# Optimization experiments

Measured on AMD Instinct MI355X. Metric: run time of the kernel, lower is better.

## Reference

```python
import jax, jax.numpy as jnp
import numpy as np

L = 8192   # sequence length
B = 4      # batch
D = 512    # embed_dim
NDIM = 16  # EMA state dim
Z = 128    # shared q/k dim
W = 128    # attention window
MP = 256   # max relative positions
NEG = -50000.0  # TOKEN_SELF_ATTN_VALUE-style mask fill


def setup_inputs() -> dict:
    key = jax.random.key(0)
    ks = jax.random.split(key, 16)
    def tn(k, shp, std):  # truncated-normal-ish init (clipped normal)
        return jnp.clip(jax.random.normal(k, shp) * std, -2 * std, 2 * std)
    val = jnp.ones((NDIM, 1)).at[1::2].set(-1.0)  # MultiHeadEMA beta init pattern
    return {
        "x": jax.random.normal(ks[0], (L, B, D), dtype=jnp.float32),
        "delta": tn(ks[1], (D, NDIM, 1), 0.2),
        "alpha": tn(ks[2], (D, NDIM, 1), 0.2),
        "beta": tn(ks[3], (D, NDIM, 1), 0.02) + val,
        "gamma": jax.random.normal(ks[4], (D, NDIM)),
        "omega": jax.random.normal(ks[5], (D,)),
        "Wp": tn(ks[6], (D, 1), 0.02),      # LatentConfigurator weight_proj
        "bp": jnp.zeros((1,)),
        "temp": jnp.array([0.5 * np.log(D)], dtype=jnp.float32),  # log(sqrt(D))
        "Wz": tn(ks[7], (D, Z), 0.02),
        "qg": jax.random.normal(ks[8], (Z,)) * 0.02 + 1.0,
        "qb": jnp.zeros((Z,)),
        "kg": jax.random.normal(ks[9], (Z,)) * 0.02 + 1.0,
        "kb": jnp.zeros((Z,)),
        "Wv": tn(ks[10], (D, D), 0.02),
        "relb": tn(ks[11], (2 * MP - 1,), 0.02),  # FastRelativePositionalBias table
    }


def _rotary(t, cos, sin):
    # t: (B, L, Z); cos/sin: (L, Z//2). Complex rotation on interleaved pairs.
    t1, t2 = t[..., 0::2], t[..., 1::2]
    return jnp.stack([t1 * cos - t2 * sin, t1 * sin + t2 * cos], axis=-1).reshape(t.shape)


def _forward(x, delta, alpha, beta, gamma, omega, Wp, bp, temp, Wz, qg, qb, kg, kb, Wv, relb):
    scale = 1.0 / np.sqrt(NDIM)
    # ---- MultiHeadEMA: damped EMA as long convolution via FFT ----
    p = jax.nn.sigmoid(delta)                      # (D,N,1)
    a = jax.nn.sigmoid(alpha)
    logq = jnp.log1p(-(p * a))                     # log(1 - p*alpha)
    t = jnp.arange(L, dtype=jnp.float32)
    kern = (p * beta) * jnp.exp(logq * t)          # (D,N,L) Vandermonde kernel
    k1d = jnp.einsum('dnl,dn->dl', kern, gamma * scale)  # (D,L)
    xb = x.transpose(1, 2, 0)                      # (B,D,L)
    conv = jnp.fft.irfft(jnp.fft.rfft(xb, n=2 * L) * jnp.fft.rfft(k1d, n=2 * L), n=2 * L)[..., :L]
    mx = jax.nn.silu(conv.transpose(2, 0, 1) + x * omega)  # (L,B,D)
    # ---- LatentConfigurator: sigmoid token routing (proj_dim==1) ----
    pi = jax.nn.sigmoid((mx @ Wp + bp) / jnp.exp(temp))[..., 0].T  # (B,L)
    mxb = mx.transpose(1, 0, 2)                    # (B,L,D)
    sel = pi > 0.5
    idx = jnp.cumsum(sel.astype(jnp.int32), axis=1) * sel  # (B,L); 0 -> dropped slot
    counts = sel.sum(axis=1)                       # (B,)
    bi = jnp.arange(B)[:, None]
    # compress_seq: scatter selected tokens to compact prefix (slot 0 dropped)
    c = jnp.zeros((B, L + 1, D), mx.dtype).at[bi, idx].add(mxb * sel[..., None])[:, 1:]
    # ---- windowed attention over compressed tokens ----
    z = jax.nn.silu(c @ Wz)                        # (B,L,Z)
    freqs = 1.0 / (10000.0 ** (jnp.arange(0, Z, 2, dtype=jnp.float32) / Z))
    ang = jnp.arange(L, dtype=jnp.float32)[:, None] * freqs
    cos, sin = jnp.cos(ang), jnp.sin(ang)
    q = _rotary(z * qg + qb, cos, sin)
    kk = _rotary(z * kg + kb, cos, sin)
    v = jax.nn.silu(c @ Wv)                        # (B,L,D)
    n = L // W
    qw = q.reshape(B, n, W, Z)
    def look_around(tw):  # prepend previous window: (B,n,W,f) -> (B,n,2W,f)
        prev = jnp.pad(tw, ((0, 0), (1, 0), (0, 0), (0, 0)))[:, :-1]
        return jnp.concatenate([prev, tw], axis=2)
    kw = look_around(kk.reshape(B, n, W, Z))
    vw = look_around(v.reshape(B, n, W, D))
    base = (jnp.arange(n) * W)[:, None, None]
    qabs = base + jnp.arange(W)[None, :, None]         # (n,W,1)
    kabs = base + jnp.arange(-W, W)[None, None, :]     # (n,1,2W)
    mask = (kabs <= qabs) & (kabs >= 0) & (kabs[None] < counts[:, None, None, None])  # (B,n,W,2W)
    rel = jnp.arange(-W, W)[None, :] - jnp.arange(W)[:, None]   # (W,2W)
    bias = relb[jnp.clip(rel + MP - 1, 0, 2 * MP - 2)]          # (W,2W)
    scores = jnp.einsum('bnwz,bnkz->bnwk', qw, kw) / np.sqrt(Z) + bias
    attn = jax.nn.softmax(jnp.where(mask, scores, NEG), axis=-1)
    h = jnp.einsum('bnwk,bnkd->bnwd', attn, vw).reshape(B, L, D)
    # ---- extract: gather back to original positions, gate by pi ----
    hpad = jnp.concatenate([jnp.zeros((B, 1, D), h.dtype), h], axis=1)
    hsel = jnp.take_along_axis(hpad, idx[..., None], axis=1)    # (B,L,D)
    return x + (hsel * pi[..., None]).transpose(1, 0, 2)        # (L,B,D)


def reference(x, delta, alpha, beta, gamma, omega, Wp, bp, temp, Wz, qg, qb, kg, kb, Wv, relb):
    return _forward(x, delta, alpha, beta, gamma, omega, Wp, bp, temp, Wz, qg, qb, kg, kb, Wv, relb)
```

## Files before the change

### kernel.cpp

```cpp
#include <hip/hip_runtime.h>
#include <math.h>

constexpr int L = 8192;
constexpr int B = 4;
constexpr int D = 512;
constexpr int NDIM = 16;
constexpr int Z = 128;
constexpr float NEGF = -50000.0f;
constexpr int CCL = 64;
constexpr int NCH = L / CCL;
constexpr int FMAX = 64;

typedef short s16x8 __attribute__((ext_vector_type(8)));
typedef float f32x4 __attribute__((ext_vector_type(4)));

typedef __attribute__((address_space(1))) const void* as1cv;
typedef __attribute__((address_space(3))) void* as3v;

__device__ __forceinline__ void gld16(const void* g, void* l) {
  __builtin_amdgcn_global_load_lds((as1cv)g, (as3v)l, 16, 0, 0);
}

__device__ __forceinline__ unsigned short f2bf(float f) {
  unsigned u = __builtin_bit_cast(unsigned, f);
  u += 0x7fffu + ((u >> 16) & 1u);
  return (unsigned short)(u >> 16);
}

__global__ __launch_bounds__(256) void k_prep(const float* __restrict__ delta,
                                              const float* __restrict__ alpha,
                                              const float* __restrict__ beta,
                                              const float* __restrict__ gamma,
                                              double* __restrict__ qdn,
                                              double* __restrict__ cdn,
                                              double* __restrict__ rp1,
                                              double* __restrict__ rp2,
                                              float* __restrict__ qf,
                                              float* __restrict__ cf,
                                              float* __restrict__ r1f,
                                              float* __restrict__ r2f,
                                              int* __restrict__ fcnt) {
  int i = blockIdx.x * 256 + threadIdx.x;
  if (i == 0) *fcnt = 0;
  if (i >= D * NDIM) return;
  double p = 1.0 / (1.0 + exp(-(double)delta[i]));
  double a = 1.0 / (1.0 + exp(-(double)alpha[i]));
  double q = 1.0 - p * a;
  double c = p * (double)beta[i] * (double)gamma[i] * 0.25;
  qdn[i] = q; cdn[i] = c;
  double q2 = q * q, q4 = q2 * q2, q8 = q4 * q4;
  double q16 = q8 * q8, q32 = q16 * q16, q64 = q32 * q32;
  rp1[i] = q64;
  rp2[i] = q64 * q64;
  qf[i] = (float)q; cf[i] = (float)c;
  r1f[i] = (float)q64; r2f[i] = (float)(q64 * q64);
}

__global__ __launch_bounds__(256) void k_convA(const float* __restrict__ x,
                                               const float* __restrict__ qf,
                                               float* __restrict__ E) {
  int bx = blockIdx.x;
  int tile = bx & 31, dg = (bx >> 5) & 7, b = bx >> 8;
  int dl = threadIdx.x & 63, cl = threadIdx.x >> 6;
  int dgl = dg * 64 + dl;
  int t = tile * 4 + cl;
  float q[NDIM], s[NDIM];
#pragma unroll
  for (int n = 0; n < NDIM; ++n) { q[n] = qf[dgl * NDIM + n]; s[n] = 0.f; }
  const float* xp = x + ((size_t)(t * CCL) * B + b) * D + dgl;
#pragma unroll 4
  for (int i = 0; i < CCL; ++i) {
    float xv = xp[i * (B * D)];
#pragma unroll
    for (int n = 0; n < NDIM; ++n) s[n] = fmaf(q[n], s[n], xv);
  }
  float* eb = E + ((size_t)(b * NCH + t) * NDIM) * 512 + dgl;
#pragma unroll
  for (int n = 0; n < NDIM; ++n) eb[(size_t)n * 512] = s[n];
}

__global__ __launch_bounds__(256) void k_convC(const float* __restrict__ x,
                                               const float* __restrict__ omega,
                                               const float* __restrict__ qf,
                                               const float* __restrict__ cf,
                                               const float* __restrict__ r1f,
                                               const float* __restrict__ r2f,
                                               const float* __restrict__ E,
                                               const float* __restrict__ Wp,
                                               unsigned short* __restrict__ mxb,
                                               float* __restrict__ pdot) {
  int bx = blockIdx.x;
  int tile = bx & 31, dg = (bx >> 5) & 7, b = bx >> 8;
  int dl = threadIdx.x & 63, cl = threadIdx.x >> 6;
  int dgl = dg * 64 + dl;
  int t = tile * 4 + cl;
  float q[NDIM], c[NDIM], s[NDIM];
#pragma unroll
  for (int n = 0; n < NDIM; ++n) {
    q[n] = qf[dgl * NDIM + n];
    c[n] = cf[dgl * NDIM + n];
    s[n] = 0.f;
  }
  if (t >= 1) {
    const float* e1 = E + ((size_t)(b * NCH + t - 1) * NDIM) * 512 + dgl;
#pragma unroll
    for (int n = 0; n < NDIM; ++n) s[n] = e1[(size_t)n * 512];
  }
  if (t >= 2) {
    const float* e2 = E + ((size_t)(b * NCH + t - 2) * NDIM) * 512 + dgl;
#pragma unroll
    for (int n = 0; n < NDIM; ++n) s[n] = fmaf(r1f[dgl * NDIM + n], e2[(size_t)n * 512], s[n]);
  }
  if (t >= 3) {
    const float* e3 = E + ((size_t)(b * NCH + t - 3) * NDIM) * 512 + dgl;
#pragma unroll
    for (int n = 0; n < NDIM; ++n) s[n] = fmaf(r2f[dgl * NDIM + n], e3[(size_t)n * 512], s[n]);
  }
  float om = omega[dgl];
  float wp = Wp[dgl];
  const float* xp = x + ((size_t)(t * CCL) * B + b) * D + dgl;
  unsigned short* mp = mxb + ((size_t)b * L + t * CCL) * 512 + dgl;
  float* pp = pdot + ((size_t)(b * L + t * CCL)) * 8 + dg;
  for (int i = 0; i < CCL; ++i) {
    float xv = xp[i * (B * D)];
#pragma unroll
    for (int n = 0; n < NDIM; ++n) s[n] = fmaf(q[n], s[n], xv);
    float p0 = c[0] * s[0], p1 = c[1] * s[1], p2 = c[2] * s[2], p3 = c[3] * s[3];
    p0 = fmaf(c[4], s[4], p0);  p1 = fmaf(c[5], s[5], p1);
    p2 = fmaf(c[6], s[6], p2);  p3 = fmaf(c[7], s[7], p3);
    p0 = fmaf(c[8], s[8], p0);  p1 = fmaf(c[9], s[9], p1);
    p2 = fmaf(c[10], s[10], p2); p3 = fmaf(c[11], s[11], p3);
    p0 = fmaf(c[12], s[12], p0); p1 = fmaf(c[13], s[13], p1);
    p2 = fmaf(c[14], s[14], p2); p3 = fmaf(c[15], s[15], p3);
    float conv = (p0 + p1) + (p2 + p3);
    float m = fmaf(xv, om, conv);
    float v = m / (1.0f + __expf(-m));
    mp[(size_t)i * 512] = f2bf(v);
    float pd = v * wp;
#pragma unroll
    for (int off = 32; off; off >>= 1) pd += __shfl_down(pd, off, 64);
    if (dl == 0) pp[(size_t)i * 8] = pd;
  }
}

__global__ __launch_bounds__(256) void k_logitc(const float* __restrict__ pdot,
                                                const float* __restrict__ bp,
                                                const float* __restrict__ temp,
                                                float* __restrict__ pi,
                                                int* __restrict__ selb,
                                                int* __restrict__ fcnt,
                                                int* __restrict__ flags) {
  int rid = blockIdx.x * 256 + threadIdx.x;
  const float* pr = pdot + (size_t)rid * 8;
  double acc = 0.0;
#pragma unroll
  for (int j = 0; j < 8; ++j) acc += (double)pr[j];
  double logit = acc + (double)bp[0];
  pi[rid] = (float)(1.0 / (1.0 + exp(-logit / exp((double)temp[0]))));
  selb[rid] = (logit > 0.0) ? 1 : 0;
  if (fabs(logit) < 1e-4) {
    int slot = atomicAdd(fcnt, 1);
    if (slot < FMAX) flags[slot] = rid;
  }
}

__global__ __launch_bounds__(256) void k_fix(const int* __restrict__ fcnt,
                                             const int* __restrict__ flags,
                                             const float* __restrict__ x,
                                             const double* __restrict__ qdn,
                                             const double* __restrict__ cdn,
                                             const double* __restrict__ rp1,
                                             const double* __restrict__ rp2,
                                             const float* __restrict__ omega,
                                             const float* __restrict__ Wp,
                                             double* __restrict__ pfix) {
  int nb = blockIdx.x;
  int fi = nb >> 3, dblk = nb & 7;
  int count = *fcnt; if (count > FMAX) count = FMAX;
  if (fi >= count) return;
  int rid = flags[fi];
  int b = rid >> 13, l = rid & (L - 1);
  int t = l >> 6, io = l & 63;
  int sub = threadIdx.x >> 6, dl = threadIdx.x & 63;
  int d = dblk * 64 + dl;
  double q[NDIM], s[NDIM];
#pragma unroll
  for (int n = 0; n < NDIM; ++n) { q[n] = qdn[d * NDIM + n]; s[n] = 0.0; }
  int c0 = (sub < 3) ? (t - 3 + sub) : t;
  int steps = (sub < 3) ? 64 : (io + 1);
  if (c0 >= 0) {
    const float* xp = x + ((size_t)(c0 * CCL) * B + b) * D + d;
    for (int i = 0; i < steps; ++i) {
      double xv = (double)xp[(size_t)i * (B * D)];
#pragma unroll
      for (int n = 0; n < NDIM; ++n) s[n] = fma(q[n], s[n], xv);
    }
  }
  __shared__ double Esm[4][64][NDIM];
#pragma unroll
  for (int n = 0; n < NDIM; ++n) Esm[sub][dl][n] = s[n];
  __syncthreads();
  if (sub == 3) {
    double sfin[NDIM];
#pragma unroll
    for (int n = 0; n < NDIM; ++n) {
      double base = q[n], r = 1.0;
      int e = io + 1;
      while (e) { if (e & 1) r *= base; base *= base; e >>= 1; }
      double S = Esm[2][dl][n] + rp1[d * NDIM + n] * Esm[1][dl][n] + rp2[d * NDIM + n] * Esm[0][dl][n];
      sfin[n] = Esm[3][dl][n] + r * S;
    }
    double conv = 0.0;
#pragma unroll
    for (int n = 0; n < NDIM; ++n) conv = fma(cdn[d * NDIM + n], sfin[n], conv);
    double xv = (double)x[((size_t)l * B + b) * D + d];
    double m = conv + xv * (double)omega[d];
    double mxd = m / (1.0 + exp(-m));
    double v = mxd * (double)Wp[d];
#pragma unroll
    for (int off = 32; off; off >>= 1) v += __shfl_down(v, off, 64);
    if (dl == 0) pfix[fi * 8 + dblk] = v;
  }
}

__global__ __launch_bounds__(64) void k_fix2(const int* __restrict__ fcnt,
                                             const int* __restrict__ flags,
                                             const double* __restrict__ pfix,
                                             const float* __restrict__ bp,
                                             const float* __restrict__ temp,
                                             float* __restrict__ pi,
                                             int* __restrict__ selb) {
  int fi = threadIdx.x;
  int count = *fcnt; if (count > FMAX) count = FMAX;
  if (fi >= count) return;
  double s = 0.0;
#pragma unroll
  for (int j = 0; j < 8; ++j) s += pfix[fi * 8 + j];
  double logit = s + (double)bp[0];
  int rid = flags[fi];
  selb[rid] = (logit > 0.0) ? 1 : 0;
  pi[rid] = (float)(1.0 / (1.0 + exp(-logit / exp((double)temp[0]))));
}

__global__ __launch_bounds__(256) void k_scan(const int* __restrict__ selb,
                                              int* __restrict__ idx,
                                              int* __restrict__ src,
                                              int* __restrict__ counts) {
  int b = blockIdx.x;
  int t = threadIdx.x;
  __shared__ int part[256];
  const int PER = L / 256;
  int base = b * L + t * PER;
  int loc[PER];
  int cnt = 0;
#pragma unroll
  for (int i = 0; i < PER; ++i) { loc[i] = selb[base + i]; cnt += loc[i]; }
  part[t] = cnt;
  __syncthreads();
  for (int off = 1; off < 256; off <<= 1) {
    int v = (t >= off) ? part[t - off] : 0;
    __syncthreads();
    part[t] += v;
    __syncthreads();
  }
  int run = (t == 0) ? 0 : part[t - 1];
#pragma unroll
  for (int i = 0; i < PER; ++i) {
    int sflag = loc[i];
    run += sflag;
    idx[base + i] = sflag ? run : 0;
    if (sflag) src[b * L + run - 1] = t * PER + i;
  }
  if (t == 255) counts[b] = part[255];
}

__global__ __launch_bounds__(256) void k_buildc(const unsigned short* __restrict__ mxb,
                                                const int* __restrict__ src,
                                                const int* __restrict__ counts,
                                                unsigned short* __restrict__ c) {
  int row = blockIdx.x * 4 + (threadIdx.x >> 6);
  int lane = threadIdx.x & 63;
  int b = row >> 13;
  int j = row & (L - 1);
  s16x8 o = {0, 0, 0, 0, 0, 0, 0, 0};
  if (j < counts[b])
    o = *(const s16x8*)(mxb + ((size_t)b * L + src[row]) * 512 + lane * 8);
  *(s16x8*)(c + (size_t)row * D + lane * 8) = o;
}

__global__ __launch_bounds__(256) void k_wt(const float* __restrict__ Wm,
                                            unsigned short* __restrict__ Wt, int N) {
  int idx = blockIdx.x * 256 + threadIdx.x;
  int n = idx >> 9, kk = idx & 511;
  Wt[idx] = f2bf(Wm[(size_t)kk * N + n]);
}

__global__ __launch_bounds__(256) void k_gemm_mfma(const unsigned short* __restrict__ A,
                                                   const unsigned short* __restrict__ Bt,
                                                   float* __restrict__ outF,
                                                   unsigned short* __restrict__ outT,
                                                   int N, int mode) {
  __shared__ char As[16384];
  __shared__ char Bs[16384];
  int tid = threadIdx.x;
  int w = tid >> 6, l = tid & 63;
  int m0 = blockIdx.x * 128, n0 = blockIdx.y * 128;
  int wr = w >> 1, wc = w & 1;
  f32x4 acc[4][4];
  f32x4 zz = {0.f, 0.f, 0.f, 0.f};
#pragma unroll
  for (int mi = 0; mi < 4; ++mi)
#pragma unroll
    for (int ni = 0; ni < 4; ++ni) acc[mi][ni] = zz;

  for (int k0 = 0; k0 < 512; k0 += 64) {
#pragma unroll
    for (int ld = 0; ld < 4; ++ld) {
      int li = w * 4 + ld;
      int row = li * 8 + (l >> 3);
      int col = (((l & 7) ^ (row & 7)) << 3);
      gld16(A + (size_t)(m0 + row) * 512 + k0 + col, As + li * 1024);
      gld16(Bt + (size_t)(n0 + row) * 512 + k0 + col, Bs + li * 1024);
    }
    __syncthreads();
    s16x8 af[4][2], bfr[4][2];
#pragma unroll
    for (int kh = 0; kh < 2; ++kh) {
#pragma unroll
      for (int mi = 0; mi < 4; ++mi) {
        int row = wr * 64 + mi * 16 + (l & 15);
        int byte = row * 128 + ((kh * 64 + ((l >> 4) * 16)) ^ ((row & 7) << 4));
        af[mi][kh] = *(const s16x8*)(As + byte);
      }
#pragma unroll
      for (int ni = 0; ni < 4; ++ni) {
        int row = wc * 64 + ni * 16 + (l & 15);
        int byte = row * 128 + ((kh * 64 + ((l >> 4) * 16)) ^ ((row & 7) << 4));
        bfr[ni][kh] = *(const s16x8*)(Bs + byte);
      }
    }
#pragma unroll
    for (int kh = 0; kh < 2; ++kh)
#pragma unroll
      for (int mi = 0; mi < 4; ++mi)
#pragma unroll
        for (int ni = 0; ni < 4; ++ni)
          acc[mi][ni] = __builtin_amdgcn_mfma_f32_16x16x32_bf16(af[mi][kh], bfr[ni][kh], acc[mi][ni], 0, 0, 0);
    __syncthreads();
  }
#pragma unroll
  for (int mi = 0; mi < 4; ++mi)
#pragma unroll
    for (int ni = 0; ni < 4; ++ni)
#pragma unroll
      for (int r = 0; r < 4; ++r) {
        float vv = acc[mi][ni][r];
        vv = vv / (1.0f + __expf(-vv));
        int mrow = m0 + wr * 64 + mi * 16 + (l >> 4) * 4 + r;
        int ncol = n0 + wc * 64 + ni * 16 + (l & 15);
        if (mode == 0) {
          outF[(size_t)mrow * N + ncol] = vv;
        } else {
          int b = mrow >> 13, j = mrow & 8191;
          outT[((size_t)(b * 512 + ncol)) * 8192 + j] = f2bf(vv);
        }
      }
}

__global__ __launch_bounds__(256) void k_rot(const float* __restrict__ z,
                                             const float* __restrict__ qg,
                                             const float* __restrict__ qb,
                                             const float* __restrict__ kg,
                                             const float* __restrict__ kb,
                                             unsigned short* __restrict__ qo,
                                             unsigned short* __restrict__ ko) {
  int tid = blockIdx.x * 256 + threadIdx.x;
  int i = tid & 63;
  int row = tid >> 6;
  int j = row & (L - 1);
  double freq = exp(((double)(-2 * i) / 128.0) * log(10000.0));
  float angf = (float)j * (float)freq;
  double sa, ca;
  sincos((double)angf, &sa, &ca);
  float cc = (float)ca, ss = (float)sa;
  size_t base = (size_t)row * Z + 2 * i;
  float z1 = z[base], z2 = z[base + 1];
  float q1 = z1 * qg[2 * i] + qb[2 * i], q2 = z2 * qg[2 * i + 1] + qb[2 * i + 1];
  float k1 = z1 * kg[2 * i] + kb[2 * i], k2 = z2 * kg[2 * i + 1] + kb[2 * i + 1];
  qo[base]     = f2bf(q1 * cc - q2 * ss);
  qo[base + 1] = f2bf(q1 * ss + q2 * cc);
  ko[base]     = f2bf(k1 * cc - k2 * ss);
  ko[base + 1] = f2bf(k1 * ss + k2 * cc);
}

__global__ __launch_bounds__(512) void k_attn_mfma(const unsigned short* __restrict__ q,
                                                   const unsigned short* __restrict__ k,
                                                   const unsigned short* __restrict__ vT,
                                                   const float* __restrict__ relb,
                                                   const int* __restrict__ counts,
                                                   float* __restrict__ h) {
  __shared__ char smem[131072];
  char* Qs = smem;
  char* Ks = smem + 32768;
  char* Ps = smem;
  char* Vs = smem + 65536;
  int tid = threadIdx.x, w = tid >> 6, l = tid & 63;
  int n = blockIdx.x & 63, b = blockIdx.x >> 6;
  int cnt = counts[b];
  int q0 = n * 128, kbase = q0 - 128;
  const size_t rowb = (size_t)b * L;

#pragma unroll
  for (int ld = 0; ld < 4; ++ld) {
    int li = w * 4 + ld;
    int row = li * 4 + (l >> 4);
    int colb = ((l & 15) * 16) ^ ((row & 7) << 4);
    gld16((const char*)(q + (rowb + q0 + row) * Z) + colb, Qs + li * 1024);
  }
#pragma unroll
  for (int ld = 0; ld < 8; ++ld) {
    int li = w * 8 + ld;
    int row = li * 4 + (l >> 4);
    int jk = kbase + row; if (jk < 0) jk = 0;
    int colb = ((l & 15) * 16) ^ ((row & 7) << 4);
    gld16((const char*)(k + (rowb + jk) * Z) + colb, Ks + li * 1024);
  }
  __syncthreads();

  int m0 = w * 16;
  f32x4 s[16];
  f32x4 zz = {0.f, 0.f, 0.f, 0.f};
#pragma unroll
  for (int ni = 0; ni < 16; ++ni) s[ni] = zz;
  s16x8 aq[4];
#pragma unroll
  for (int ks = 0; ks < 4; ++ks) {
    int row = m0 + (l & 15);
    int byte = row * 256 + ((ks * 64 + ((l >> 4) * 16)) ^ ((row & 7) << 4));
    aq[ks] = *(const s16x8*)(Qs + byte);
  }
#pragma unroll
  for (int ni = 0; ni < 16; ++ni) {
    int row = ni * 16 + (l & 15);
    int rb = row * 256, sw = (row & 7) << 4;
#pragma unroll
    for (int ks = 0; ks < 4; ++ks) {
      s16x8 bk = *(const s16x8*)(Ks + rb + ((ks * 64 + ((l >> 4) * 16)) ^ sw));
      s[ni] = __builtin_amdgcn_mfma_f32_16x16x32_bf16(aq[ks], bk, s[ni], 0, 0, 0);
    }
  }
  __syncthreads();

  auto stageV = [&](int nc) {
#pragma unroll
    for (int ld = 0; ld < 8; ++ld) {
      int li = w * 8 + ld;
      int row = li * 2 + (l >> 5);
      int colb = ((l & 31) * 16) ^ ((row & 7) << 4);
      int j = kbase + (colb >> 1);
      if (j < 0) j = 0;
      gld16((const char*)(vT + ((size_t)(b * 512 + nc * 128 + row)) * L + j), Vs + li * 1024);
    }
  };
  stageV(0);

  int rgrp = (l >> 4) * 4;
  float mxr[4] = {-3e38f, -3e38f, -3e38f, -3e38f};
#pragma unroll
  for (int ni = 0; ni < 16; ++ni) {
    int col = ni * 16 + (l & 15);
    int kabs = kbase + col;
#pragma unroll
    for (int r = 0; r < 4; ++r) {
      int ww = m0 + rgrp + r;
      bool valid = (kabs >= 0) && (kabs <= q0 + ww) && (kabs < cnt);
      float vv = valid ? (s[ni][r] * 0.08838834764831845f + relb[col + 127 - ww]) : NEGF;
      s[ni][r] = vv;
      mxr[r] = fmaxf(mxr[r], vv);
    }
  }
#pragma unroll
  for (int r = 0; r < 4; ++r)
    for (int off = 1; off < 16; off <<= 1)
      mxr[r] = fmaxf(mxr[r], __shfl_xor(mxr[r], off, 64));
  float smr[4] = {0.f, 0.f, 0.f, 0.f};
#pragma unroll
  for (int ni = 0; ni < 16; ++ni)
#pragma unroll
    for (int r = 0; r < 4; ++r) {
      float p = __expf(s[ni][r] - mxr[r]);
      s[ni][r] = p;
      smr[r] += p;
    }
#pragma unroll
  for (int r = 0; r < 4; ++r) {
    for (int off = 1; off < 16; off <<= 1) smr[r] += __shfl_xor(smr[r], off, 64);
    smr[r] = 1.0f / smr[r];
  }
#pragma unroll
  for (int ni = 0; ni < 16; ++ni) {
    int colb2 = (ni * 16 + (l & 15)) * 2;
#pragma unroll
    for (int r = 0; r < 4; ++r) {
      int row = m0 + rgrp + r;
      *(unsigned short*)(Ps + row * 512 + (colb2 ^ ((row & 7) << 4))) = f2bf(s[ni][r] * smr[r]);
    }
  }
  __syncthreads();

  for (int nc = 0; nc < 4; ++nc) {
    if (nc) {
      __syncthreads();
      stageV(nc);
      __syncthreads();
    }
    f32x4 o[8];
#pragma unroll
    for (int ni = 0; ni < 8; ++ni) o[ni] = zz;
    int prow = m0 + (l & 15);
    int psw = (prow & 7) << 4;
#pragma unroll
    for (int kt = 0; kt < 4; ++kt) {
      s16x8 pa0 = *(const s16x8*)(Ps + prow * 512 + ((kt * 128 + ((l >> 4) * 16)) ^ psw));
      s16x8 pa1 = *(const s16x8*)(Ps + prow * 512 + ((kt * 128 + 64 + ((l >> 4) * 16)) ^ psw));
#pragma unroll
      for (int ni = 0; ni < 8; ++ni) {
        int vrow = ni * 16 + (l & 15);
        int vsw = (vrow & 7) << 4;
        s16x8 vb0 = *(const s16x8*)(Vs + vrow * 512 + ((kt * 128 + ((l >> 4) * 16)) ^ vsw));
        s16x8 vb1 = *(const s16x8*)(Vs + vrow * 512 + ((kt * 128 + 64 + ((l >> 4) * 16)) ^ vsw));
        o[ni] = __builtin_amdgcn_mfma_f32_16x16x32_bf16(pa0, vb0, o[ni], 0, 0, 0);
        o[ni] = __builtin_amdgcn_mfma_f32_16x16x32_bf16(pa1, vb1, o[ni], 0, 0, 0);
      }
    }
#pragma unroll
    for (int ni = 0; ni < 8; ++ni)
#pragma unroll
      for (int r = 0; r < 4; ++r)
        h[(rowb + q0 + m0 + rgrp + r) * 512 + nc * 128 + ni * 16 + (l & 15)] = o[ni][r];
  }
}

__global__ __launch_bounds__(256) void k_final(const float* __restrict__ x,
                                               const float* __restrict__ h,
                                               const float* __restrict__ pi,
                                               const int* __restrict__ idx,
                                               float* __restrict__ out) {
  int e4 = blockIdx.x * 256 + threadIdx.x;
  int dq = e4 & 127;
  int rem = e4 >> 7;
  int b = rem & 3;
  int l = rem >> 2;
  float4 xv = ((const float4*)x)[e4];
  int ix = idx[(b << 13) + l];
  if (ix > 0) {
    float pv = pi[(b << 13) + l];
    float4 hv = ((const float4*)(h + ((size_t)(b << 13) + ix - 1) * 512))[dq];
    xv.x += hv.x * pv; xv.y += hv.y * pv;
    xv.z += hv.z * pv; xv.w += hv.w * pv;
  }
  ((float4*)out)[e4] = xv;
}

extern "C" void kernel_launch(void* const* d_in, const int* in_sizes, int n_in,
                              void* d_out, int out_size, void* d_ws, size_t ws_size,
                              hipStream_t stream) {
  const float* x     = (const float*)d_in[0];
  const float* delta = (const float*)d_in[1];
  const float* alpha = (const float*)d_in[2];
  const float* beta  = (const float*)d_in[3];
  const float* gamma = (const float*)d_in[4];
  const float* omega = (const float*)d_in[5];
  const float* Wp    = (const float*)d_in[6];
  const float* bp    = (const float*)d_in[7];
  const float* temp  = (const float*)d_in[8];
  const float* Wz    = (const float*)d_in[9];
  const float* qg    = (const float*)d_in[10];
  const float* qb    = (const float*)d_in[11];
  const float* kg    = (const float*)d_in[12];
  const float* kb    = (const float*)d_in[13];
  const float* Wv    = (const float*)d_in[14];
  const float* relb  = (const float*)d_in[15];
  (void)in_sizes; (void)n_in; (void)out_size; (void)ws_size;

  char* wsb = (char*)d_ws;
  size_t o = 0;
  auto alloc = [&](size_t bytes) {
    char* p = wsb + o;
    o += (bytes + 255) & ~(size_t)255;
    return p;
  };
  float* hbuf          = (float*)alloc((size_t)B * L * D * 4);
  unsigned short* mxb  = (unsigned short*)hbuf;
  char*  eAndCb        = alloc((size_t)B * L * D * 2);
  float* Ebuf          = (float*)eAndCb;
  unsigned short* cb   = (unsigned short*)eAndCb;
  float* zb            = (float*)alloc((size_t)B * L * Z * 4);
  unsigned short* qb2  = (unsigned short*)alloc((size_t)B * L * Z * 2);
  unsigned short* kb2  = (unsigned short*)alloc((size_t)B * L * Z * 2);
  unsigned short* vTb  = (unsigned short*)alloc((size_t)B * D * L * 2);
  unsigned short* wzt  = (unsigned short*)alloc((size_t)Z * 512 * 2);
  unsigned short* wvt  = (unsigned short*)alloc((size_t)D * 512 * 2);
  float* pdot = (float*)alloc((size_t)B * L * 8 * 4);
  float* pib  = (float*)alloc((size_t)B * L * 4);
  int* selb   = (int*)alloc((size_t)B * L * 4);
  int* idx    = (int*)alloc((size_t)B * L * 4);
  int* src    = (int*)alloc((size_t)B * L * 4);
  int* cnt    = (int*)alloc(256);
  double* qdn = (double*)alloc((size_t)D * NDIM * 8);
  double* cdn = (double*)alloc((size_t)D * NDIM * 8);
  double* rp1 = (double*)alloc((size_t)D * NDIM * 8);
  double* rp2 = (double*)alloc((size_t)D * NDIM * 8);
  float* qf   = (float*)alloc((size_t)D * NDIM * 4);
  float* cf   = (float*)alloc((size_t)D * NDIM * 4);
  float* r1f  = (float*)alloc((size_t)D * NDIM * 4);
  float* r2f  = (float*)alloc((size_t)D * NDIM * 4);
  int* fcnt   = (int*)alloc(256);
  int* flags  = (int*)alloc(FMAX * 4);
  double* pfix = (double*)alloc((size_t)FMAX * 8 * 8);

  k_prep<<<(D * NDIM + 255) / 256, 256, 0, stream>>>(delta, alpha, beta, gamma,
                                                     qdn, cdn, rp1, rp2, qf, cf, r1f, r2f, fcnt);
  k_convA<<<B * 8 * 32, 256, 0, stream>>>(x, qf, Ebuf);
  k_convC<<<B * 8 * 32, 256, 0, stream>>>(x, omega, qf, cf, r1f, r2f, Ebuf, Wp, mxb, pdot);
  k_logitc<<<B * L / 256, 256, 0, stream>>>(pdot, bp, temp, pib, selb, fcnt, flags);
  k_fix<<<FMAX * 8, 256, 0, stream>>>(fcnt, flags, x, qdn, cdn, rp1, rp2, omega, Wp, pfix);
  k_fix2<<<1, 64, 0, stream>>>(fcnt, flags, pfix, bp, temp, pib, selb);
  k_scan<<<B, 256, 0, stream>>>(selb, idx, src, cnt);
  k_buildc<<<B * L / 4, 256, 0, stream>>>(mxb, src, cnt, cb);
  k_wt<<<Z * 512 / 256, 256, 0, stream>>>(Wz, wzt, Z);
  k_wt<<<D * 512 / 256, 256, 0, stream>>>(Wv, wvt, D);
  k_gemm_mfma<<<dim3(256, 1), 256, 0, stream>>>(cb, wzt, zb, vTb, Z, 0);
  k_gemm_mfma<<<dim3(256, 4), 256, 0, stream>>>(cb, wvt, zb, vTb, D, 1);
  k_rot<<<B * L * (Z / 2) / 256, 256, 0, stream>>>(zb, qg, qb, kg, kb, qb2, kb2);
  k_attn_mfma<<<B * 64, 512, 0, stream>>>(qb2, kb2, vTb, relb, cnt, hbuf);
  k_final<<<(int)((size_t)L * B * D / 4 / 256), 256, 0, stream>>>(x, hbuf, pib, idx, (float*)d_out);
}
```

Before: 272.2 us.

## Fuse gather into GEMM, tabulate rotary, DPP reduction, LDS-transposed stores

Removes the k_buildc gather kernel and its intermediate buffer. The GEMM now loads A rows directly from mxb through the src index, and k_scan zero-fills the unused src entries. The transposed bf16 V output is staged through swizzled LDS so global writes are 16-byte coalesced. Rotary cos/sin are computed once per position in a small table kernel instead of a double-precision sincos per batch element. The per-step 64-lane shuffle reduction in convC becomes a DPP reduction, with an unroll added. Padded rows now compute on real row-0 data instead of zeros, which is safe only if those rows stay masked downstream.

Result: faster. 230.2 us (-15.4%).

```diff
diff --git a/kernel.cpp b/kernel.cpp
--- a/kernel.cpp
+++ b/kernel.cpp
@@ -26,6 +26,13 @@
   u += 0x7fffu + ((u >> 16) & 1u);
   return (unsigned short)(u >> 16);
 }
+
+#define DPPADD(acc, ctrl, rmask)                                                   \
+  {                                                                                \
+    int _mv = __builtin_amdgcn_update_dpp(0, __builtin_bit_cast(int, acc),         \
+                                          ctrl, rmask, 0xf, false);                \
+    acc += __builtin_bit_cast(float, _mv);                                         \
+  }
 
 __global__ __launch_bounds__(256) void k_prep(const float* __restrict__ delta,
                                               const float* __restrict__ alpha,
@@ -56,6 +63,17 @@
   r1f[i] = (float)q64; r2f[i] = (float)(q64 * q64);
 }
 
+__global__ __launch_bounds__(256) void k_tab(float2* __restrict__ tab) {
+  int tid = blockIdx.x * 256 + threadIdx.x;
+  int i = tid & 63, j = tid >> 6;
+  double freq = exp(((double)(-2 * i) / 128.0) * log(10000.0));
+  float angf = (float)j * (float)freq;
+  double sa, ca;
+  sincos((double)angf, &sa, &ca);
+  float2 r; r.x = (float)ca; r.y = (float)sa;
+  tab[tid] = r;
+}
+
 __global__ __launch_bounds__(256) void k_convA(const float* __restrict__ x,
                                                const float* __restrict__ qf,
                                                float* __restrict__ E) {
@@ -121,6 +139,7 @@
   const float* xp = x + ((size_t)(t * CCL) * B + b) * D + dgl;
   unsigned short* mp = mxb + ((size_t)b * L + t * CCL) * 512 + dgl;
   float* pp = pdot + ((size_t)(b * L + t * CCL)) * 8 + dg;
+#pragma unroll 4
   for (int i = 0; i < CCL; ++i) {
     float xv = xp[i * (B * D)];
 #pragma unroll
@@ -137,9 +156,13 @@
     float v = m / (1.0f + __expf(-m));
     mp[(size_t)i * 512] = f2bf(v);
     float pd = v * wp;
-#pragma unroll
-    for (int off = 32; off; off >>= 1) pd += __shfl_down(pd, off, 64);
-    if (dl == 0) pp[(size_t)i * 8] = pd;
+    DPPADD(pd, 0x111, 0xf);
+    DPPADD(pd, 0x112, 0xf);
+    DPPADD(pd, 0x114, 0xf);
+    DPPADD(pd, 0x118, 0xf);
+    DPPADD(pd, 0x142, 0xa);
+    DPPADD(pd, 0x143, 0x8);
+    if (dl == 63) pp[(size_t)i * 8] = pd;
   }
 }
 
@@ -272,20 +295,9 @@
     if (sflag) src[b * L + run - 1] = t * PER + i;
   }
   if (t == 255) counts[b] = part[255];
-}
-
-__global__ __launch_bounds__(256) void k_buildc(const unsigned short* __restrict__ mxb,
-                                                const int* __restrict__ src,
-                                                const int* __restrict__ counts,
-                                                unsigned short* __restrict__ c) {
-  int row = blockIdx.x * 4 + (threadIdx.x >> 6);
-  int lane = threadIdx.x & 63;
-  int b = row >> 13;
-  int j = row & (L - 1);
-  s16x8 o = {0, 0, 0, 0, 0, 0, 0, 0};
-  if (j < counts[b])
-    o = *(const s16x8*)(mxb + ((size_t)b * L + src[row]) * 512 + lane * 8);
-  *(s16x8*)(c + (size_t)row * D + lane * 8) = o;
+  __syncthreads();
+  int total = part[255];
+  for (int i2 = total + t; i2 < L; i2 += 256) src[b * L + i2] = 0;
 }
 
 __global__ __launch_bounds__(256) void k_wt(const float* __restrict__ Wm,
@@ -295,17 +307,31 @@
   Wt[idx] = f2bf(Wm[(size_t)kk * N + n]);
 }
 
-__global__ __launch_bounds__(256) void k_gemm_mfma(const unsigned short* __restrict__ A,
+__global__ __launch_bounds__(256) void k_gemm_mfma(const unsigned short* __restrict__ mxb,
+                                                   const int* __restrict__ src,
                                                    const unsigned short* __restrict__ Bt,
                                                    float* __restrict__ outF,
                                                    unsigned short* __restrict__ outT,
                                                    int N, int mode) {
-  __shared__ char As[16384];
-  __shared__ char Bs[16384];
+  __shared__ char smem[32768];
+  char* As = smem;
+  char* Bs = smem + 16384;
   int tid = threadIdx.x;
   int w = tid >> 6, l = tid & 63;
   int m0 = blockIdx.x * 128, n0 = blockIdx.y * 128;
+  int gb = m0 >> 13, j0 = m0 & 8191;
   int wr = w >> 1, wc = w & 1;
+  const unsigned short* arow[4];
+  const unsigned short* brow[4];
+#pragma unroll
+  for (int ld = 0; ld < 4; ++ld) {
+    int li = w * 4 + ld;
+    int row = li * 8 + (l >> 3);
+    int col = ((l & 7) ^ (row & 7)) << 3;
+    int srow = src[gb * 8192 + j0 + row];
+    arow[ld] = mxb + ((size_t)gb * 8192 + srow) * 512 + col;
+    brow[ld] = Bt + (size_t)(n0 + row) * 512 + col;
+  }
   f32x4 acc[4][4];
   f32x4 zz = {0.f, 0.f, 0.f, 0.f};
 #pragma unroll
@@ -317,10 +343,8 @@
 #pragma unroll
     for (int ld = 0; ld < 4; ++ld) {
       int li = w * 4 + ld;
-      int row = li * 8 + (l >> 3);
-      int col = (((l & 7) ^ (row & 7)) << 3);
-      gld16(A + (size_t)(m0 + row) * 512 + k0 + col, As + li * 1024);
-      gld16(Bt + (size_t)(n0 + row) * 512 + k0 + col, Bs + li * 1024);
+      gld16(arow[ld] + k0, As + li * 1024);
+      gld16(brow[ld] + k0, Bs + li * 1024);
     }
     __syncthreads();
     s16x8 af[4][2], bfr[4][2];
@@ -348,26 +372,49 @@
           acc[mi][ni] = __builtin_amdgcn_mfma_f32_16x16x32_bf16(af[mi][kh], bfr[ni][kh], acc[mi][ni], 0, 0, 0);
     __syncthreads();
   }
-#pragma unroll
-  for (int mi = 0; mi < 4; ++mi)
-#pragma unroll
-    for (int ni = 0; ni < 4; ++ni)
-#pragma unroll
-      for (int r = 0; r < 4; ++r) {
-        float vv = acc[mi][ni][r];
-        vv = vv / (1.0f + __expf(-vv));
-        int mrow = m0 + wr * 64 + mi * 16 + (l >> 4) * 4 + r;
-        int ncol = n0 + wc * 64 + ni * 16 + (l & 15);
-        if (mode == 0) {
+  if (mode == 0) {
+#pragma unroll
+    for (int mi = 0; mi < 4; ++mi)
+#pragma unroll
+      for (int ni = 0; ni < 4; ++ni)
+#pragma unroll
+        for (int r = 0; r < 4; ++r) {
+          float vv = acc[mi][ni][r];
+          vv = vv / (1.0f + __expf(-vv));
+          int mrow = m0 + wr * 64 + mi * 16 + (l >> 4) * 4 + r;
+          int ncol = n0 + wc * 64 + ni * 16 + (l & 15);
           outF[(size_t)mrow * N + ncol] = vv;
-        } else {
-          int b = mrow >> 13, j = mrow & 8191;
-          outT[((size_t)(b * 512 + ncol)) * 8192 + j] = f2bf(vv);
         }
-      }
+  } else {
+    unsigned short* ts = (unsigned short*)smem;
+    (void)ts;
+#pragma unroll
+    for (int mi = 0; mi < 4; ++mi)
+#pragma unroll
+      for (int ni = 0; ni < 4; ++ni)
+#pragma unroll
+        for (int r = 0; r < 4; ++r) {
+          float vv = acc[mi][ni][r];
+          vv = vv / (1.0f + __expf(-vv));
+          int mrow = wr * 64 + mi * 16 + (l >> 4) * 4 + r;
+          int ncol = wc * 64 + ni * 16 + (l & 15);
+          int byteoff = ncol * 256 + ((mrow * 2) ^ ((ncol & 7) << 4));
+          *(unsigned short*)(smem + byteoff) = f2bf(vv);
+        }
+    __syncthreads();
+#pragma unroll
+    for (int it = 0; it < 8; ++it) {
+      int ncol = w * 32 + it * 4 + (l >> 4);
+      int ch = l & 15;
+      int byteoff = ncol * 256 + ((ch * 16) ^ ((ncol & 7) << 4));
+      s16x8 vch = *(const s16x8*)(smem + byteoff);
+      *(s16x8*)(outT + ((size_t)(gb * 512 + n0 + ncol)) * 8192 + j0 + ch * 8) = vch;
+    }
+  }
 }
 
 __global__ __launch_bounds__(256) void k_rot(const float* __restrict__ z,
+                                             const float2* __restrict__ tab,
                                              const float* __restrict__ qg,
                                              const float* __restrict__ qb,
                                              const float* __restrict__ kg,
@@ -378,11 +425,8 @@
   int i = tid & 63;
   int row = tid >> 6;
   int j = row & (L - 1);
-  double freq = exp(((double)(-2 * i) / 128.0) * log(10000.0));
-  float angf = (float)j * (float)freq;
-  double sa, ca;
-  sincos((double)angf, &sa, &ca);
-  float cc = (float)ca, ss = (float)sa;
+  float2 cs = tab[j * 64 + i];
+  float cc = cs.x, ss = cs.y;
   size_t base = (size_t)row * Z + 2 * i;
   float z1 = z[base], z2 = z[base + 1];
   float q1 = z1 * qg[2 * i] + qb[2 * i], q2 = z2 * qg[2 * i + 1] + qb[2 * i + 1];
@@ -592,15 +636,14 @@
   };
   float* hbuf          = (float*)alloc((size_t)B * L * D * 4);
   unsigned short* mxb  = (unsigned short*)hbuf;
-  char*  eAndCb        = alloc((size_t)B * L * D * 2);
-  float* Ebuf          = (float*)eAndCb;
-  unsigned short* cb   = (unsigned short*)eAndCb;
+  float* Ebuf          = (float*)((char*)hbuf + (size_t)B * L * D * 2);
   float* zb            = (float*)alloc((size_t)B * L * Z * 4);
   unsigned short* qb2  = (unsigned short*)alloc((size_t)B * L * Z * 2);
   unsigned short* kb2  = (unsigned short*)alloc((size_t)B * L * Z * 2);
   unsigned short* vTb  = (unsigned short*)alloc((size_t)B * D * L * 2);
   unsigned short* wzt  = (unsigned short*)alloc((size_t)Z * 512 * 2);
   unsigned short* wvt  = (unsigned short*)alloc((size_t)D * 512 * 2);
+  float2* tab = (float2*)alloc((size_t)L * 64 * 8);
   float* pdot = (float*)alloc((size_t)B * L * 8 * 4);
   float* pib  = (float*)alloc((size_t)B * L * 4);
   int* selb   = (int*)alloc((size_t)B * L * 4);
@@ -621,18 +664,18 @@
 
   k_prep<<<(D * NDIM + 255) / 256, 256, 0, stream>>>(delta, alpha, beta, gamma,
                                                      qdn, cdn, rp1, rp2, qf, cf, r1f, r2f, fcnt);
+  k_tab<<<L * 64 / 256, 256, 0, stream>>>(tab);
   k_convA<<<B * 8 * 32, 256, 0, stream>>>(x, qf, Ebuf);
   k_convC<<<B * 8 * 32, 256, 0, stream>>>(x, omega, qf, cf, r1f, r2f, Ebuf, Wp, mxb, pdot);
   k_logitc<<<B * L / 256, 256, 0, stream>>>(pdot, bp, temp, pib, selb, fcnt, flags);
   k_fix<<<FMAX * 8, 256, 0, stream>>>(fcnt, flags, x, qdn, cdn, rp1, rp2, omega, Wp, pfix);
   k_fix2<<<1, 64, 0, stream>>>(fcnt, flags, pfix, bp, temp, pib, selb);
   k_scan<<<B, 256, 0, stream>>>(selb, idx, src, cnt);
-  k_buildc<<<B * L / 4, 256, 0, stream>>>(mxb, src, cnt, cb);
   k_wt<<<Z * 512 / 256, 256, 0, stream>>>(Wz, wzt, Z);
   k_wt<<<D * 512 / 256, 256, 0, stream>>>(Wv, wvt, D);
-  k_gemm_mfma<<<dim3(256, 1), 256, 0, stream>>>(cb, wzt, zb, vTb, Z, 0);
-  k_gemm_mfma<<<dim3(256, 4), 256, 0, stream>>>(cb, wvt, zb, vTb, D, 1);
-  k_rot<<<B * L * (Z / 2) / 256, 256, 0, stream>>>(zb, qg, qb, kg, kb, qb2, kb2);
+  k_gemm_mfma<<<dim3(256, 1), 256, 0, stream>>>(mxb, src, wzt, zb, vTb, Z, 0);
+  k_gemm_mfma<<<dim3(256, 4), 256, 0, stream>>>(mxb, src, wvt, zb, vTb, D, 1);
+  k_rot<<<B * L * (Z / 2) / 256, 256, 0, stream>>>(zb, tab, qg, qb, kg, kb, qb2, kb2);
   k_attn_mfma<<<B * 64, 512, 0, stream>>>(qb2, kb2, vTb, relb, cnt, hbuf);
   k_final<<<(int)((size_t)L * B * D / 4 / 256), 256, 0, stream>>>(x, hbuf, pib, idx, (float*)d_out);
 }
```
